# Kernel optimization log

Measured on AMD Instinct MI355X. Metric: run time of the kernel, lower is better.

The kernel has to match this reference:

```python
import jax, jax.numpy as jnp
import numpy as np


def lstm_cell(carry, x, Wx, Wh, b):
    # carry = (h, c), x: [B, E]; standard fused-gate LSTM
    h, c = carry
    z = x @ Wx + h @ Wh + b  # [B, 4U]
    i, f, g, o = jnp.split(z, 4, axis=-1)
    c = jax.nn.sigmoid(f) * c + jax.nn.sigmoid(i) * jnp.tanh(g)
    h = jax.nn.sigmoid(o) * jnp.tanh(c)
    return (h, c)


def run_lstm(xs, Wx, Wh, b, units):
    # xs: [T, B, E] -> final hidden state [B, U]
    B = xs.shape[1]
    init = (jnp.zeros((B, units), xs.dtype), jnp.zeros((B, units), xs.dtype))
    def step(carry, x):
        carry = lstm_cell(carry, x, Wx, Wh, b)
        return carry, None
    (h, _), _ = jax.lax.scan(step, init, xs)
    return h


def setup_inputs() -> dict:
    key = jax.random.key(0)
    ks = jax.random.split(key, 12)
    B, T, V, E, U = 64, 512, 50000, 256, 512
    s = lambda *d: 1.0 / np.sqrt(d[0])
    return {
        "sentence": jax.random.randint(ks[0], (B, T), 0, V, dtype=jnp.int32),
        "emb": jax.random.normal(ks[1], (V, E), jnp.float32) * 0.02,
        "Wx_f": jax.random.normal(ks[2], (E, 4 * U), jnp.float32) * s(E),
        "Wh_f": jax.random.normal(ks[3], (U, 4 * U), jnp.float32) * s(U),
        "b_f": jnp.zeros((4 * U,), jnp.float32),
        "Wx_b": jax.random.normal(ks[4], (E, 4 * U), jnp.float32) * s(E),
        "Wh_b": jax.random.normal(ks[5], (U, 4 * U), jnp.float32) * s(U),
        "b_b": jnp.zeros((4 * U,), jnp.float32),
        "W1": jax.random.normal(ks[6], (2 * U, 64), jnp.float32) * s(2 * U),
        "b1": jnp.zeros((64,), jnp.float32),
        "W2": jax.random.normal(ks[7], (64, 1), jnp.float32) * s(64),
        "b2": jnp.zeros((1,), jnp.float32),
    }


def reference(sentence, emb, Wx_f, Wh_f, b_f, Wx_b, Wh_b, b_b, W1, b1, W2, b2):
    U = Wh_f.shape[0]
    x = emb[sentence]                      # [B, T, E]
    xs = jnp.swapaxes(x, 0, 1)             # [T, B, E]
    h_fwd = run_lstm(xs, Wx_f, Wh_f, b_f, U)           # forward direction
    h_bwd = run_lstm(xs[::-1], Wx_b, Wh_b, b_b, U)     # backward direction
    h = jnp.concatenate([h_fwd, h_bwd], axis=1)        # [B, 2U]
    hidden = h @ W1 + b1                    # Dense(64), linear
    return jax.nn.sigmoid(hidden @ W2 + b2) # Dense(1, sigmoid)
```

## Files before the change

### kernel.cpp

```cpp
#include <hip/hip_runtime.h>
#include <hip/hip_bf16.h>

typedef __bf16 bf16x8 __attribute__((ext_vector_type(8)));
typedef float f32x4 __attribute__((ext_vector_type(4)));
typedef unsigned int u32;
typedef unsigned short u16;
typedef unsigned long long u64;

#define T_ 512
#define E_ 256
#define U_ 512

static const size_t WS_XS = 0;
static const size_t WS_W2 = (size_t)16 << 20;
static const size_t WS_HP = WS_W2 + 6291456;
static const size_t WS_HF = WS_HP + 524288;

__device__ __forceinline__ float fsigm(float x) { return 1.f / (1.f + __expf(-x)); }
__device__ __forceinline__ float ftanh(float x) {
  float e = __expf(2.f * fabsf(x));
  float r = 1.f - 2.f / (e + 1.f);
  return copysignf(r, x);
}

__global__ void embed_swz_kernel(const int* __restrict__ sent,
                                 const float* __restrict__ emb,
                                 __bf16* __restrict__ xs_g) {
  int id = blockIdx.x * 256 + threadIdx.x;
  int gx = id & 31;
  int b  = (id >> 5) & 63;
  int t  = id >> 11;
  int idx = sent[b * T_ + t];
  const float* src = emb + (size_t)idx * E_ + gx * 8;
  bf16x8 v;
#pragma unroll
  for (int j = 0; j < 8; ++j) v[j] = (__bf16)src[j];
  int gs = gx ^ (b & 7);
  *(bf16x8*)(xs_g + (size_t)(t * 64 + b) * E_ + gs * 8) = v;
}

__global__ void __launch_bounds__(256)
wprep_kernel(const float* __restrict__ Wx_f, const float* __restrict__ Wh_f,
             const float* __restrict__ Wx_b, const float* __restrict__ Wh_b,
             __bf16* __restrict__ w2, u32* __restrict__ hpub) {
  int bid = blockIdx.x;
  int tid = threadIdx.x;
  {
    int zid = bid * 256 + tid;
    if (zid < 131072) hpub[zid] = 0u;
  }
  int jg = bid % 6;
  int wv = (bid / 6) & 7;
  int us = (bid / 48) & 15;
  int d  = bid / 768;
  int j    = jg * 4 + (tid >> 6);
  int lane = tid & 63;
  int c    = wv * 16 + (lane & 15);
  int ul   = c >> 2, gate = c & 3;
  int n    = gate * 512 + us * 32 + ul;
  int k0   = j * 32 + (lane >> 4) * 8;
  const float* Wx = d ? Wx_b : Wx_f;
  const float* Wh = d ? Wh_b : Wh_f;
  bf16x8 v;
#pragma unroll
  for (int e = 0; e < 8; ++e) {
    int k = k0 + e;
    float f = (k < 256) ? Wx[(size_t)k * 2048 + n] : Wh[(size_t)(k - 256) * 2048 + n];
    v[e] = (__bf16)f;
  }
  size_t og = ((size_t)((d * 16 + us) * 8 + wv) * 24 + j) * 64 + lane;
  *(bf16x8*)(w2 + og * 8) = v;
}

__global__ void __launch_bounds__(512)
lstm_main(const __bf16* __restrict__ xs_g, const __bf16* __restrict__ w2,
          u32* __restrict__ hpub, float* __restrict__ hfin,
          const float* __restrict__ b_f, const float* __restrict__ b_b) {
  __shared__ __align__(16) __bf16 xbuf[2][16 * 256];
  __shared__ __align__(16) __bf16 hbuf[16 * 512];

  const int wg   = blockIdx.x;
  const int dir  = wg >> 6;
  const int sl   = wg & 63;
  const int us   = sl >> 2;
  const int q    = sl & 3;
  const int tid  = threadIdx.x;
  const int wv   = tid >> 6;
  const int lane = tid & 63;
  const int bq_l = lane & 15;
  const int kq   = lane >> 4;
  const int bsw  = bq_l & 7;
  const int ul_own = wv * 4 + kq;
  const int u_own  = us * 32 + ul_own;
  const int b_own  = q * 16 + bq_l;

  bf16x8 wfrag[24];
  {
    const bf16x8* wp = (const bf16x8*)w2 +
                       ((size_t)((dir * 16 + us) * 8 + wv) * 24) * 64 + lane;
#pragma unroll
    for (int j = 0; j < 24; ++j) wfrag[j] = wp[j * 64];
  }

  const float* bias = dir ? b_b : b_f;
  const float bi  = bias[u_own];
  const float bff = bias[512 + u_own];
  const float bg  = bias[1024 + u_own];
  const float bo  = bias[1536 + u_own];
  float c_st = 0.f;

  u32* const pw0 = hpub + ((size_t)(dir * 2 + 0) * 64 + q * 16 + us) * 512 + wv * 64 + lane;
  u32* const pw1 = pw0 + 32768;

  const int us_p  = 2 * wv + (lane >> 5);
  const int lane5 = lane & 31;
  const u64* const cs0 = (const u64*)(hpub + ((size_t)(dir * 2 + 0) * 64 + q * 16 + us_p) * 512) + lane5;
  const u64* const cs1 = cs0 + 16384;
  const int cc = lane5 >> 3;
  const int cb0 = 2 * (lane5 & 7);
  const int cb1 = cb0 + 1;
  int cd0[8], cd1[8];
#pragma unroll
  for (int j = 0; j < 8; ++j) {
    int u = us_p * 32 + j * 4 + cc;
    int g = u >> 3;
    cd0[j] = cb0 * 1024 + ((g ^ (cb0 & 7)) << 4) + ((u & 7) << 1);
    cd1[j] = cb1 * 1024 + ((g ^ (cb1 & 7)) << 4) + ((u & 7) << 1);
  }

  {
    int t0 = dir ? (T_ - 1) : 0;
    const uint4* xsrc = (const uint4*)(xs_g + ((size_t)t0 * 64 + q * 16) * 256);
    ((uint4*)xbuf[0])[tid] = xsrc[tid];
  }
  __syncthreads();

  for (int t = 0;; ++t) {
    const bool lastt = (t == T_ - 1);
    u64 v[8];
    const u64* csrc = (t & 1) ? cs1 : cs0;
    if (t > 0) {
#pragma unroll
      for (int j = 0; j < 8; ++j)
        v[j] = __hip_atomic_load(csrc + j * 32, __ATOMIC_RELAXED, __HIP_MEMORY_SCOPE_AGENT);
    }
    uint4 xg;
    if (!lastt) {
      const int teff = dir ? (T_ - 2 - t) : (t + 1);
      xg = ((const uint4*)(xs_g + ((size_t)teff * 64 + q * 16) * 256))[tid];
    }

    f32x4 acc0 = {0.f, 0.f, 0.f, 0.f};
    f32x4 acc1 = {0.f, 0.f, 0.f, 0.f};
    const __bf16* xb = xbuf[t & 1];
#pragma unroll
    for (int j = 0; j < 8; ++j) {
      int g = j * 4 + kq;
      bf16x8 a = *(const bf16x8*)(xb + bq_l * 256 + ((g ^ bsw) << 3));
      if (j & 1) acc1 = __builtin_amdgcn_mfma_f32_16x16x32_bf16(wfrag[j], a, acc1, 0, 0, 0);
      else       acc0 = __builtin_amdgcn_mfma_f32_16x16x32_bf16(wfrag[j], a, acc0, 0, 0, 0);
    }

    if (t > 0) {
      const u32 ep = (u32)t;
      for (;;) {
        u32 bad = 0;
#pragma unroll
        for (int j = 0; j < 8; ++j)
          bad |= ((u32)v[j] ^ ep) | ((u32)(v[j] >> 32) ^ ep);
        bad &= 0xFFFFu;
        if (!__any((int)bad)) break;
        __builtin_amdgcn_s_sleep(1);
#pragma unroll
        for (int j = 0; j < 8; ++j)
          v[j] = __hip_atomic_load(csrc + j * 32, __ATOMIC_RELAXED, __HIP_MEMORY_SCOPE_AGENT);
      }
#pragma unroll
      for (int j = 0; j < 8; ++j) {
        *(u16*)((char*)hbuf + cd0[j]) = (u16)(v[j] >> 16);
        *(u16*)((char*)hbuf + cd1[j]) = (u16)(v[j] >> 48);
      }
      __syncthreads();
#pragma unroll
      for (int j = 0; j < 16; ++j) {
        int g = j * 4 + kq;
        bf16x8 a = *(const bf16x8*)(hbuf + bq_l * 512 + ((g ^ bsw) << 3));
        if (j & 1) acc1 = __builtin_amdgcn_mfma_f32_16x16x32_bf16(wfrag[8 + j], a, acc1, 0, 0, 0);
        else       acc0 = __builtin_amdgcn_mfma_f32_16x16x32_bf16(wfrag[8 + j], a, acc0, 0, 0, 0);
      }
    }

    const float zi = acc0[0] + acc1[0] + bi;
    const float zf = acc0[1] + acc1[1] + bff;
    const float zg = acc0[2] + acc1[2] + bg;
    const float zo = acc0[3] + acc1[3] + bo;
    c_st = fsigm(zf) * c_st + fsigm(zi) * ftanh(zg);
    const float hv = fsigm(zo) * ftanh(c_st);

    if (lastt) {
      hfin[(size_t)dir * 32768 + b_own * 512 + u_own] = hv;
      break;
    }

    {
      union { __bf16 h; u16 s; } cv;
      cv.h = (__bf16)hv;
      u32 word = ((u32)cv.s << 16) | (u32)(t + 1);
      __hip_atomic_store(((t + 1) & 1) ? pw1 : pw0, word, __ATOMIC_RELAXED,
                         __HIP_MEMORY_SCOPE_AGENT);
    }
    ((uint4*)xbuf[(t + 1) & 1])[tid] = xg;
    __syncthreads();
  }
}

__global__ void __launch_bounds__(1024)
dense_kernel(const float* __restrict__ hfin, const float* __restrict__ W1,
             const float* __restrict__ b1, const float* __restrict__ W2,
             const float* __restrict__ b2, float* __restrict__ out) {
  __shared__ float hid[64][64];
  const int t = threadIdx.x;
  const int b = t >> 4;
  const int jg = t & 15;
  float a0 = b1[jg * 4 + 0], a1 = b1[jg * 4 + 1], a2 = b1[jg * 4 + 2], a3 = b1[jg * 4 + 3];
#pragma unroll 8
  for (int k = 0; k < 1024; ++k) {
    const float hv = hfin[(size_t)(k >> 9) * 32768 + b * 512 + (k & 511)];
    const float4 w = *(const float4*)(W1 + (size_t)k * 64 + jg * 4);
    a0 += hv * w.x; a1 += hv * w.y; a2 += hv * w.z; a3 += hv * w.w;
  }
  hid[b][jg * 4 + 0] = a0; hid[b][jg * 4 + 1] = a1;
  hid[b][jg * 4 + 2] = a2; hid[b][jg * 4 + 3] = a3;
  __syncthreads();
  if (t < 64) {
    float l = b2[0];
#pragma unroll 8
    for (int j = 0; j < 64; ++j) l += hid[t][j] * W2[j];
    out[t] = 1.f / (1.f + __expf(-l));
  }
}

extern "C" void kernel_launch(void* const* d_in, const int* in_sizes, int n_in,
                              void* d_out, int out_size, void* d_ws, size_t ws_size,
                              hipStream_t stream) {
  const int*   sent = (const int*)d_in[0];
  const float* emb  = (const float*)d_in[1];
  const float* Wx_f = (const float*)d_in[2];
  const float* Wh_f = (const float*)d_in[3];
  const float* b_f  = (const float*)d_in[4];
  const float* Wx_b = (const float*)d_in[5];
  const float* Wh_b = (const float*)d_in[6];
  const float* b_b  = (const float*)d_in[7];
  const float* W1   = (const float*)d_in[8];
  const float* b1   = (const float*)d_in[9];
  const float* W2   = (const float*)d_in[10];
  const float* b2   = (const float*)d_in[11];
  float* out = (float*)d_out;

  char* ws = (char*)d_ws;
  __bf16* xs_g = (__bf16*)(ws + WS_XS);
  __bf16* w2   = (__bf16*)(ws + WS_W2);
  u32*    hpub = (u32*)(ws + WS_HP);
  float*  hfin = (float*)(ws + WS_HF);

  hipLaunchKernelGGL(embed_swz_kernel, dim3(4096), dim3(256), 0, stream, sent, emb, xs_g);
  hipLaunchKernelGGL(wprep_kernel, dim3(1536), dim3(256), 0, stream,
                     Wx_f, Wh_f, Wx_b, Wh_b, w2, hpub);

  void* args[] = {(void*)&xs_g, (void*)&w2, (void*)&hpub, (void*)&hfin,
                  (void*)&b_f, (void*)&b_b};
  hipLaunchCooperativeKernel((void*)lstm_main, dim3(128), dim3(512), args, 0, stream);

  hipLaunchKernelGGL(dense_kernel, dim3(1), dim3(1024), 0, stream,
                     hfin, W1, b1, W2, b2, out);
}
```

Baseline: 1.308 ms.

## Fuse prep kernels, remap workgroups, use inline-asm polling loads, parallelize dense head

Merges the embedding gather and weight-prep kernels into a single launch. Remaps LSTM workgroup ids so the direction and batch-quarter come from the low bits, which changes how blocks are placed across CUs and XCDs. Replaces the per-step atomic polling loads with an inline-asm batch of sc0 global loads and an explicit waitcnt, and swaps __syncthreads for a raw s_barrier. The dense head now runs over 64 blocks instead of one. The asm path depends on sc0 loads seeing the other workgroups' stores coherently, which adds memory-ordering risk.

Measured after the change: 1.084 ms, median of 2. 17.1% less time.

```diff
diff --git a/kernel.cpp b/kernel.cpp
--- a/kernel.cpp
+++ b/kernel.cpp
@@ -23,28 +23,28 @@
   return copysignf(r, x);
 }
 
-__global__ void embed_swz_kernel(const int* __restrict__ sent,
-                                 const float* __restrict__ emb,
-                                 __bf16* __restrict__ xs_g) {
-  int id = blockIdx.x * 256 + threadIdx.x;
-  int gx = id & 31;
-  int b  = (id >> 5) & 63;
-  int t  = id >> 11;
-  int idx = sent[b * T_ + t];
-  const float* src = emb + (size_t)idx * E_ + gx * 8;
-  bf16x8 v;
-#pragma unroll
-  for (int j = 0; j < 8; ++j) v[j] = (__bf16)src[j];
-  int gs = gx ^ (b & 7);
-  *(bf16x8*)(xs_g + (size_t)(t * 64 + b) * E_ + gs * 8) = v;
-}
-
 __global__ void __launch_bounds__(256)
-wprep_kernel(const float* __restrict__ Wx_f, const float* __restrict__ Wh_f,
-             const float* __restrict__ Wx_b, const float* __restrict__ Wh_b,
-             __bf16* __restrict__ w2, u32* __restrict__ hpub) {
-  int bid = blockIdx.x;
-  int tid = threadIdx.x;
+prep_kernel(const int* __restrict__ sent, const float* __restrict__ emb,
+            __bf16* __restrict__ xs_g,
+            const float* __restrict__ Wx_f, const float* __restrict__ Wh_f,
+            const float* __restrict__ Wx_b, const float* __restrict__ Wh_b,
+            __bf16* __restrict__ w2, u32* __restrict__ hpub) {
+  const int tid = threadIdx.x;
+  if (blockIdx.x < 4096) {
+    int id = blockIdx.x * 256 + tid;
+    int gx = id & 31;
+    int b  = (id >> 5) & 63;
+    int t  = id >> 11;
+    int idx = sent[b * T_ + t];
+    const float* src = emb + (size_t)idx * E_ + gx * 8;
+    bf16x8 v;
+#pragma unroll
+    for (int j = 0; j < 8; ++j) v[j] = (__bf16)src[j];
+    int gs = gx ^ (b & 7);
+    *(bf16x8*)(xs_g + (size_t)(t * 64 + b) * E_ + gs * 8) = v;
+    return;
+  }
+  int bid = blockIdx.x - 4096;
   {
     int zid = bid * 256 + tid;
     if (zid < 131072) hpub[zid] = 0u;
@@ -80,10 +80,10 @@
   __shared__ __align__(16) __bf16 hbuf[16 * 512];
 
   const int wg   = blockIdx.x;
-  const int dir  = wg >> 6;
-  const int sl   = wg & 63;
-  const int us   = sl >> 2;
-  const int q    = sl & 3;
+  const int q7   = wg & 7;
+  const int dir  = q7 >> 2;
+  const int q    = q7 & 3;
+  const int us   = wg >> 3;
   const int tid  = threadIdx.x;
   const int wv   = tid >> 6;
   const int lane = tid & 63;
@@ -109,12 +109,13 @@
   const float bo  = bias[1536 + u_own];
   float c_st = 0.f;
 
-  u32* const pw0 = hpub + ((size_t)(dir * 2 + 0) * 64 + q * 16 + us) * 512 + wv * 64 + lane;
-  u32* const pw1 = pw0 + 32768;
+  u32* const pw0 = hpub + ((size_t)(((dir * 2 + 0) * 4 + q) * 16 + us)) * 512 +
+                   wv * 64 + lane;
 
   const int us_p  = 2 * wv + (lane >> 5);
   const int lane5 = lane & 31;
-  const u64* const cs0 = (const u64*)(hpub + ((size_t)(dir * 2 + 0) * 64 + q * 16 + us_p) * 512) + lane5;
+  const u64* const cs0 = (const u64*)(hpub +
+      ((size_t)(((dir * 2 + 0) * 4 + q) * 16 + us_p)) * 512) + lane5;
   const u64* const cs1 = cs0 + 16384;
   const int cc = lane5 >> 3;
   const int cb0 = 2 * (lane5 & 7);
@@ -140,9 +141,20 @@
     u64 v[8];
     const u64* csrc = (t & 1) ? cs1 : cs0;
     if (t > 0) {
-#pragma unroll
-      for (int j = 0; j < 8; ++j)
-        v[j] = __hip_atomic_load(csrc + j * 32, __ATOMIC_RELAXED, __HIP_MEMORY_SCOPE_AGENT);
+      asm volatile(
+          "global_load_dwordx2 %[o0], %[a], off sc0\n\t"
+          "global_load_dwordx2 %[o1], %[a], off offset:256 sc0\n\t"
+          "global_load_dwordx2 %[o2], %[a], off offset:512 sc0\n\t"
+          "global_load_dwordx2 %[o3], %[a], off offset:768 sc0\n\t"
+          "global_load_dwordx2 %[o4], %[a], off offset:1024 sc0\n\t"
+          "global_load_dwordx2 %[o5], %[a], off offset:1280 sc0\n\t"
+          "global_load_dwordx2 %[o6], %[a], off offset:1536 sc0\n\t"
+          "global_load_dwordx2 %[o7], %[a], off offset:1792 sc0"
+          : [o0] "=&v"(v[0]), [o1] "=&v"(v[1]), [o2] "=&v"(v[2]),
+            [o3] "=&v"(v[3]), [o4] "=&v"(v[4]), [o5] "=&v"(v[5]),
+            [o6] "=&v"(v[6]), [o7] "=&v"(v[7])
+          : [a] "v"(csrc)
+          : "memory");
     }
     uint4 xg;
     if (!lastt) {
@@ -162,6 +174,8 @@
     }
 
     if (t > 0) {
+      asm volatile("s_waitcnt vmcnt(0)" ::: "memory");
+      __builtin_amdgcn_sched_barrier(0);
       const u32 ep = (u32)t;
       for (;;) {
         u32 bad = 0;
@@ -180,7 +194,10 @@
         *(u16*)((char*)hbuf + cd0[j]) = (u16)(v[j] >> 16);
         *(u16*)((char*)hbuf + cd1[j]) = (u16)(v[j] >> 48);
       }
-      __syncthreads();
+      asm volatile("s_waitcnt lgkmcnt(0)" ::: "memory");
+      __builtin_amdgcn_sched_barrier(0);
+      __builtin_amdgcn_s_barrier();
+      __builtin_amdgcn_sched_barrier(0);
 #pragma unroll
       for (int j = 0; j < 16; ++j) {
         int g = j * 4 + kq;
@@ -206,7 +223,7 @@
       union { __bf16 h; u16 s; } cv;
       cv.h = (__bf16)hv;
       u32 word = ((u32)cv.s << 16) | (u32)(t + 1);
-      __hip_atomic_store(((t + 1) & 1) ? pw1 : pw0, word, __ATOMIC_RELAXED,
+      __hip_atomic_store(pw0 + ((t + 1) & 1) * 32768, word, __ATOMIC_RELAXED,
                          __HIP_MEMORY_SCOPE_AGENT);
     }
     ((uint4*)xbuf[(t + 1) & 1])[tid] = xg;
@@ -214,29 +231,32 @@
   }
 }
 
-__global__ void __launch_bounds__(1024)
+__global__ void __launch_bounds__(256)
 dense_kernel(const float* __restrict__ hfin, const float* __restrict__ W1,
              const float* __restrict__ b1, const float* __restrict__ W2,
              const float* __restrict__ b2, float* __restrict__ out) {
-  __shared__ float hid[64][64];
-  const int t = threadIdx.x;
-  const int b = t >> 4;
-  const int jg = t & 15;
-  float a0 = b1[jg * 4 + 0], a1 = b1[jg * 4 + 1], a2 = b1[jg * 4 + 2], a3 = b1[jg * 4 + 3];
-#pragma unroll 8
-  for (int k = 0; k < 1024; ++k) {
+  __shared__ float part[4][64];
+  __shared__ float hw[64];
+  const int b   = blockIdx.x;
+  const int tid = threadIdx.x;
+  const int kc  = tid >> 6;
+  const int j   = tid & 63;
+  float a = (kc == 0) ? b1[j] : 0.f;
+#pragma unroll 4
+  for (int k = kc * 256; k < kc * 256 + 256; ++k) {
     const float hv = hfin[(size_t)(k >> 9) * 32768 + b * 512 + (k & 511)];
-    const float4 w = *(const float4*)(W1 + (size_t)k * 64 + jg * 4);
-    a0 += hv * w.x; a1 += hv * w.y; a2 += hv * w.z; a3 += hv * w.w;
-  }
-  hid[b][jg * 4 + 0] = a0; hid[b][jg * 4 + 1] = a1;
-  hid[b][jg * 4 + 2] = a2; hid[b][jg * 4 + 3] = a3;
+    a += hv * W1[(size_t)k * 64 + j];
+  }
+  part[kc][j] = a;
   __syncthreads();
-  if (t < 64) {
+  if (tid < 64)
+    hw[tid] = (part[0][tid] + part[1][tid] + part[2][tid] + part[3][tid]) * W2[tid];
+  __syncthreads();
+  if (tid == 0) {
     float l = b2[0];
 #pragma unroll 8
-    for (int j = 0; j < 64; ++j) l += hid[t][j] * W2[j];
-    out[t] = 1.f / (1.f + __expf(-l));
+    for (int i = 0; i < 64; ++i) l += hw[i];
+    out[b] = 1.f / (1.f + __expf(-l));
   }
 }
 
@@ -263,14 +283,13 @@
   u32*    hpub = (u32*)(ws + WS_HP);
   float*  hfin = (float*)(ws + WS_HF);
 
-  hipLaunchKernelGGL(embed_swz_kernel, dim3(4096), dim3(256), 0, stream, sent, emb, xs_g);
-  hipLaunchKernelGGL(wprep_kernel, dim3(1536), dim3(256), 0, stream,
-                     Wx_f, Wh_f, Wx_b, Wh_b, w2, hpub);
+  hipLaunchKernelGGL(prep_kernel, dim3(5632), dim3(256), 0, stream,
+                     sent, emb, xs_g, Wx_f, Wh_f, Wx_b, Wh_b, w2, hpub);
 
   void* args[] = {(void*)&xs_g, (void*)&w2, (void*)&hpub, (void*)&hfin,
                   (void*)&b_f, (void*)&b_b};
   hipLaunchCooperativeKernel((void*)lstm_main, dim3(128), dim3(512), args, 0, stream);
 
-  hipLaunchKernelGGL(dense_kernel, dim3(1), dim3(1024), 0, stream,
+  hipLaunchKernelGGL(dense_kernel, dim3(64), dim3(256), 0, stream,
                      hfin, W1, b1, W2, b2, out);
 }
```
